# Optimization experiments

Measured on AMD Instinct MI355X. Metric: run time of the kernel, lower is better.

## Reference

```python
import jax, jax.numpy as jnp
import numpy as np

N_IN, AUX = 768, 255
NVARS = N_IN + 1 + AUX  # 1024
K, B = 32, 64
MAX_ITER = 10
PROX_LAM = 0.01


def _build_full(z, is_input):
    b = z.shape[0]
    z_full = jnp.concatenate([jnp.ones((b, 1), z.dtype), z, jnp.zeros((b, AUX), z.dtype)], axis=1)
    ii = jnp.concatenate([jnp.ones((b, 1), is_input.dtype), is_input, jnp.zeros((b, AUX), is_input.dtype)], axis=1)
    return z_full, ii


def _init_V(key, z_full, is_input_full):
    # v0: per-batch unit 'truth' direction; inputs start at -cos(pi z) v0 + sin(pi z) r
    k1, k2 = jax.random.split(key)
    v0 = jax.random.normal(k1, (B, K), jnp.float32)
    v0 = v0 / jnp.linalg.norm(v0, axis=-1, keepdims=True)
    R = jax.random.normal(k2, (B, NVARS, K), jnp.float32)
    R = R - jnp.einsum('bnk,bk->bn', R, v0)[..., None] * v0[:, None, :]
    R = R / jnp.linalg.norm(R, axis=-1, keepdims=True)  # unit, orthogonal to v0
    c = jnp.cos(jnp.pi * z_full)[..., None]
    s = jnp.sin(jnp.pi * z_full)[..., None]
    V = jnp.where(is_input_full[..., None] > 0, -c * v0[:, None, :] + s * R, R)
    V = V.at[:, 0].set(v0)  # truth variable (z=1)
    return V, v0, R


def _mix_solve(C, V, free):
    # sequential coordinate descent (Mixing method): v_i <- -g_i/||g_i||, g_i = C[i] @ V
    def step(Vc, i):
        g = jnp.einsum('j,bjk->bk', C[i], Vc)  # C_ii = 0 excludes self
        gn = jnp.maximum(jnp.linalg.norm(g, axis=-1, keepdims=True), 1e-12)
        v = jnp.where(free[:, i][:, None], -g / gn, Vc[:, i])
        return Vc.at[:, i].set(v), None

    def sweep(_, Vc):
        Vc, _ = jax.lax.scan(step, Vc, jnp.arange(1, NVARS))
        return Vc

    return jax.lax.fori_loop(0, MAX_ITER, sweep, V)


def _forward(C, z, is_input):
    z_full, ii = _build_full(z, is_input)
    free = ii == 0
    V, v0, R = _init_V(jax.random.key(42), z_full, ii)
    V = _mix_solve(C, V, free)
    cosang = jnp.clip(-jnp.einsum('bnk,bk->bn', V, v0), -1.0 + 1e-7, 1.0 - 1e-7)
    z_out = jnp.where(free, jnp.arccos(cosang) / jnp.pi, z_full)
    return z_out[:, 1:NVARS - AUX], (z_full, ii, free, V, v0, R)


def setup_inputs() -> dict:
    key = jax.random.key(0)
    kc, kz, ki = jax.random.split(key, 3)
    Ct = jax.random.normal(kc, (NVARS, NVARS), jnp.float32)
    Ct = Ct + Ct.T - 1.0
    Ct = Ct * (1.0 - jnp.eye(NVARS, dtype=jnp.float32))  # zero diagonal
    Ct = Ct * (0.5 / (NVARS * 2)) ** 0.5  # weight_normalize
    z = jax.random.uniform(kz, (B, N_IN), jnp.float32)
    is_input = jax.random.randint(ki, (B, N_IN), 0, 2).astype(jnp.int32)
    return {"C": Ct, "z": z, "is_input": is_input}


def reference(C, z, is_input):
    out, _ = _forward(C, z, is_input)
    return out
```

## Files before the change

### kernel.cpp

```cpp
#include <hip/hip_runtime.h>
#include <stdint.h>
#include <math.h>

#define NVARS 1024
#define KDIM 32
#define BATCH 64
#define NIN 768
#define MAXIT 10

#define SMEM_BYTES 156096

typedef float f32x2 __attribute__((ext_vector_type(2)));

#define PKSETUP(A0v, A1v, Dv)                                                  \
    const float4 A0_ = (A0v), A1_ = (A1v), d_ = (Dv);                          \
    f32x2 c01, c23, c45, c67, dx_, dy_, dz_, dw_;                              \
    c01.x = A0_.x; c01.y = A0_.y; c23.x = A0_.z; c23.y = A0_.w;                \
    c45.x = A1_.x; c45.y = A1_.y; c67.x = A1_.z; c67.y = A1_.w;                \
    dx_.x = d_.x;  dx_.y = d_.x;  dy_.x = d_.y;  dy_.y = d_.y;                 \
    dz_.x = d_.z;  dz_.y = d_.z;  dw_.x = d_.w;  dw_.y = d_.w;

#define PKG0                                                                   \
    Q0_0 = __builtin_elementwise_fma(c01, dx_, Q0_0);                          \
    Q1_0 = __builtin_elementwise_fma(c01, dy_, Q1_0);                          \
    Q2_0 = __builtin_elementwise_fma(c01, dz_, Q2_0);                          \
    Q3_0 = __builtin_elementwise_fma(c01, dw_, Q3_0);
#define PKG1                                                                   \
    Q0_1 = __builtin_elementwise_fma(c23, dx_, Q0_1);                          \
    Q1_1 = __builtin_elementwise_fma(c23, dy_, Q1_1);                          \
    Q2_1 = __builtin_elementwise_fma(c23, dz_, Q2_1);                          \
    Q3_1 = __builtin_elementwise_fma(c23, dw_, Q3_1);
#define PKG2                                                                   \
    Q0_2 = __builtin_elementwise_fma(c45, dx_, Q0_2);                          \
    Q1_2 = __builtin_elementwise_fma(c45, dy_, Q1_2);                          \
    Q2_2 = __builtin_elementwise_fma(c45, dz_, Q2_2);                          \
    Q3_2 = __builtin_elementwise_fma(c45, dw_, Q3_2);
#define PKG3                                                                   \
    Q0_3 = __builtin_elementwise_fma(c67, dx_, Q0_3);                          \
    Q1_3 = __builtin_elementwise_fma(c67, dy_, Q1_3);                          \
    Q2_3 = __builtin_elementwise_fma(c67, dz_, Q2_3);                          \
    Q3_3 = __builtin_elementwise_fma(c67, dw_, Q3_3);

#define PKROWR(A0v, A1v, Dv, Ra, Rb, Rc, Rd)                                   \
  { PKSETUP(A0v, A1v, Dv) PKG##Ra PKG##Rb PKG##Rc PKG##Rd }

#define PKROW(A0v, A1v, Dv) PKROWR(A0v, A1v, Dv, 0, 1, 2, 3)

__device__ __forceinline__ void tf2x32(uint32_t key0, uint32_t key1,
                                       uint32_t& x0, uint32_t& x1) {
  uint32_t ks2 = key0 ^ key1 ^ 0x1BD11BDAu;
  x0 += key0; x1 += key1;
#define TFR(r) { x0 += x1; x1 = (x1 << r) | (x1 >> (32 - r)); x1 ^= x0; }
  TFR(13) TFR(15) TFR(26) TFR(6)
  x0 += key1; x1 += ks2 + 1u;
  TFR(17) TFR(29) TFR(16) TFR(24)
  x0 += ks2;  x1 += key0 + 2u;
  TFR(13) TFR(15) TFR(26) TFR(6)
  x0 += key0; x1 += key1 + 3u;
  TFR(17) TFR(29) TFR(16) TFR(24)
  x0 += key1; x1 += ks2 + 4u;
  TFR(13) TFR(15) TFR(26) TFR(6)
  x0 += ks2;  x1 += key0 + 5u;
#undef TFR
}

__device__ __forceinline__ uint32_t pbits(uint32_t k0, uint32_t k1, uint32_t flat) {
  uint32_t x0 = 0u, x1 = flat;
  tf2x32(k0, k1, x0, x1);
  return x0 ^ x1;
}

__device__ __forceinline__ float erfinv_xla(float x) {
  float w = -log1pf(-x * x);
  float p;
  if (w < 5.0f) {
    w -= 2.5f;
    p = 2.81022636e-08f;
    p = fmaf(p, w, 3.43273939e-07f);
    p = fmaf(p, w, -3.5233877e-06f);
    p = fmaf(p, w, -4.39150654e-06f);
    p = fmaf(p, w, 0.00021858087f);
    p = fmaf(p, w, -0.00125372503f);
    p = fmaf(p, w, -0.00417768164f);
    p = fmaf(p, w, 0.246640727f);
    p = fmaf(p, w, 1.50140941f);
  } else {
    w = sqrtf(w) - 3.0f;
    p = -0.000200214257f;
    p = fmaf(p, w, 0.000100950558f);
    p = fmaf(p, w, 0.00134934322f);
    p = fmaf(p, w, -0.00367342844f);
    p = fmaf(p, w, 0.00573950773f);
    p = fmaf(p, w, -0.0076224613f);
    p = fmaf(p, w, 0.00943887047f);
    p = fmaf(p, w, 1.00167406f);
    p = fmaf(p, w, 2.83297682f);
  }
  return p * x;
}

__device__ __forceinline__ float bits_to_normal(uint32_t bits) {
  uint32_t fb = (bits >> 9) | 0x3F800000u;
  float f = __uint_as_float(fb) - 1.0f;
  const float lo = -0.99999994f;
  float u = fmaf(f, 2.0f, lo);
  u = fmaxf(lo, u);
  return 1.41421356237f * erfinv_xla(u);
}

__device__ __forceinline__ double red32d(double v) {
  v += __shfl_xor(v, 16);
  v += __shfl_xor(v, 8);
  v += __shfl_xor(v, 4);
  v += __shfl_xor(v, 2);
  v += __shfl_xor(v, 1);
  return v;
}

__device__ __forceinline__ int pop64(uint64_t& b) {
  if (b == 0ull) return -1;
  int i = (int)__builtin_ctzll(b);
  b &= b - 1ull;
  return i;
}

template <int CTRL>
__device__ __forceinline__ float dppadd(float s) {
  int v = __builtin_amdgcn_update_dpp(0, __float_as_int(s), CTRL, 0xF, 0xF, true);
  return s + __int_as_float(v);
}

#define PROW(iiL, mL, pL, cL, Ra, Rb, Rc, Rd)                                  \
  {                                                                            \
    const bool on = ((iiL) < 32) ? ((myLo >> (iiL)) & 1u)                      \
                                 : ((myHi >> ((iiL) - 32)) & 1u);              \
    if (on) {                                                                  \
      const int row = base + (iiL);                                            \
      float4 c0 = *(const float4*)(Cd + (iiL) * 64 + 8 * jgR);                 \
      float4 c1 = *(const float4*)(Cd + (iiL) * 64 + 8 * jgR + 4);             \
      float4 vold = *(const float4*)(Vs + row * 32 + 4 * kg);                  \
      const float g0 = (Q0_##pL).cL, g1 = (Q1_##pL).cL;                        \
      const float g2 = (Q2_##pL).cL, g3 = (Q3_##pL).cL;                        \
      float s = g0 * g0;                                                       \
      s = fmaf(g1, g1, s); s = fmaf(g2, g2, s); s = fmaf(g3, g3, s);           \
      s = dppadd<0xB1>(s);                   \
      s = dppadd<0x4E>(s);                   \
      s = dppadd<0x141>(s);                  \
      const float sc = fmaxf(s, 1e-24f);                                       \
      const float inv = -__builtin_amdgcn_rsqf(sc);                            \
      float4 vnew, d;                                                          \
      vnew.x = g0 * inv; d.x = vnew.x - vold.x;                                \
      vnew.y = g1 * inv; d.y = vnew.y - vold.y;                                \
      vnew.z = g2 * inv; d.z = vnew.z - vold.z;                                \
      vnew.w = g3 * inv; d.w = vnew.w - vold.w;                                \
      if (jgR == (mL)) *(float4*)(dVs + n * 32 + 4 * kg) = d;                  \
      asm volatile("" ::: "memory");                \
      if (lane == 0) progV[spar] = n + 1;                                      \
      float4 dd = *(const float4*)(dVs + n * 32 + 4 * kg);                     \
      if (jgR == (mL)) *(float4*)(Vs + row * 32 + 4 * kg) = vnew;              \
      PKROWR(c0, c1, dd, Ra, Rb, Rc, Rd);                                      \
      ++n;                                                                     \
    }                                                                          \
  }

#define PGRP(mL)                                                               \
  PROW(8 * (mL) + 0, mL, 0, x, 0, 1, 2, 3)                                     \
  PROW(8 * (mL) + 1, mL, 0, y, 1, 2, 3, 0)                                     \
  PROW(8 * (mL) + 2, mL, 1, x, 1, 2, 3, 0)                                     \
  PROW(8 * (mL) + 3, mL, 1, y, 2, 3, 0, 1)                                     \
  PROW(8 * (mL) + 4, mL, 2, x, 2, 3, 0, 1)                                     \
  PROW(8 * (mL) + 5, mL, 2, y, 3, 0, 1, 2)                                     \
  PROW(8 * (mL) + 6, mL, 3, x, 3, 0, 1, 2)                                     \
  PROW(8 * (mL) + 7, mL, 3, y, 0, 1, 2, 3)

__global__ __launch_bounds__(1024, 4) void mixnet_kernel(
    const float* __restrict__ C32, const float* __restrict__ zin,
    const int* __restrict__ is_in, float* __restrict__ out) {
  extern __shared__ char smemraw[];
  float*    Vs    = (float*)smemraw;
  float*    Cd    = (float*)(smemraw + 131072);
  float*    dVs   = (float*)(smemraw + 147456);
  uint32_t* fmask = (uint32_t*)(smemraw + 155648);
  double*   v0D   = (double*)(smemraw + 155776);
  volatile int* progV = (volatile int*)(smemraw + 156032);

  const int tid  = threadIdx.x;
  const int b    = blockIdx.x;
  const int jg   = tid >> 3;
  const int kg   = tid & 7;
  const int lane = tid & 63;
  const int wave = tid >> 6;
  const int jgR  = jg & 7;

  uint32_t myLo, myHi;
  {
    int row = tid;
    bool fr;
    if (row == 0) fr = false;
    else if (row <= NIN) fr = (is_in[b * NIN + row - 1] == 0);
    else fr = true;
    unsigned long long m = __ballot(fr);
    myLo = (uint32_t)m; myHi = (uint32_t)(m >> 32);
    if (lane == 0) { fmask[2 * wave] = myLo; fmask[2 * wave + 1] = myHi; }
  }
  if (tid == 0) { progV[0] = 0; progV[1] = 0; }

  uint32_t a0 = 0u, a1 = 0u; tf2x32(0u, 42u, a0, a1);
  uint32_t b0 = 0u, b1 = 1u; tf2x32(0u, 42u, b0, b1);

  if (tid < 32) {
    float raw = bits_to_normal(pbits(a0, a1, (uint32_t)(b * KDIM + tid)));
    double n2 = red32d((double)raw * (double)raw);
    v0D[tid] = (double)raw / sqrt(n2);
  }
  __syncthreads();

  const double PI_D = 3.14159265358979323846;

  {
    double vrow[32];
    if (tid == 0) {
#pragma unroll
      for (int t = 0; t < 16; ++t) {
        double2 w = *(const double2*)(v0D + 2 * t);
        vrow[2 * t] = w.x; vrow[2 * t + 1] = w.y;
      }
    } else {
      uint32_t base = ((uint32_t)(b * NVARS + tid)) * KDIM;
#pragma unroll
      for (int q = 0; q < 32; ++q)
        vrow[q] = (double)bits_to_normal(pbits(b0, b1, base + (uint32_t)q));
      double dot = 0.0;
#pragma unroll
      for (int t = 0; t < 16; ++t) {
        double2 w = *(const double2*)(v0D + 2 * t);
        dot += vrow[2 * t] * w.x + vrow[2 * t + 1] * w.y;
      }
#pragma unroll
      for (int t = 0; t < 16; ++t) {
        double2 w = *(const double2*)(v0D + 2 * t);
        vrow[2 * t]     -= dot * w.x;
        vrow[2 * t + 1] -= dot * w.y;
      }
      double n2 = 0.0;
#pragma unroll
      for (int q = 0; q < 32; ++q) n2 += vrow[q] * vrow[q];
      double rinv = 1.0 / sqrt(n2);
#pragma unroll
      for (int q = 0; q < 32; ++q) vrow[q] *= rinv;
      if (tid <= NIN && is_in[b * NIN + tid - 1] > 0) {
        double zf = (double)zin[b * NIN + tid - 1];
        double cc = cos(PI_D * zf), sn = sin(PI_D * zf);
#pragma unroll
        for (int t = 0; t < 16; ++t) {
          double2 w = *(const double2*)(v0D + 2 * t);
          vrow[2 * t]     = -cc * w.x + sn * vrow[2 * t];
          vrow[2 * t + 1] = -cc * w.y + sn * vrow[2 * t + 1];
        }
      }
    }
#pragma unroll
    for (int q = 0; q < 8; ++q) {
      float4 w;
      w.x = (float)vrow[4 * q];     w.y = (float)vrow[4 * q + 1];
      w.z = (float)vrow[4 * q + 2]; w.w = (float)vrow[4 * q + 3];
      *(float4*)(Vs + tid * 32 + 4 * q) = w;
    }
  }
  __syncthreads();

  f32x2 Q0_0, Q1_0, Q2_0, Q3_0, Q0_1, Q1_1, Q2_1, Q3_1;
  f32x2 Q0_2, Q1_2, Q2_2, Q3_2, Q0_3, Q1_3, Q2_3, Q3_3;
  {
    float Gj[32];
#pragma unroll
    for (int q = 0; q < 32; ++q) Gj[q] = 0.f;
    const float* Cb = C32 + (size_t)(8 * jg) * NVARS;
    for (int i = 0; i < NVARS; i += 4) {
      float4 cw[8];
#pragma unroll
      for (int l = 0; l < 8; ++l)
        cw[l] = *(const float4*)(Cb + (size_t)l * NVARS + i);
#pragma unroll
      for (int u = 0; u < 4; ++u) {
        float4 vv = *(const float4*)(Vs + (i + u) * 32 + 4 * kg);
#pragma unroll
        for (int l = 0; l < 8; ++l) {
          float cu = (u == 0) ? cw[l].x : (u == 1) ? cw[l].y
                   : (u == 2) ? cw[l].z : cw[l].w;
          Gj[l * 4 + 0] = fmaf(cu, vv.x, Gj[l * 4 + 0]);
          Gj[l * 4 + 1] = fmaf(cu, vv.y, Gj[l * 4 + 1]);
          Gj[l * 4 + 2] = fmaf(cu, vv.z, Gj[l * 4 + 2]);
          Gj[l * 4 + 3] = fmaf(cu, vv.w, Gj[l * 4 + 3]);
        }
      }
    }
    Q0_0.x = Gj[0];  Q0_0.y = Gj[4];  Q1_0.x = Gj[1];  Q1_0.y = Gj[5];
    Q2_0.x = Gj[2];  Q2_0.y = Gj[6];  Q3_0.x = Gj[3];  Q3_0.y = Gj[7];
    Q0_1.x = Gj[8];  Q0_1.y = Gj[12]; Q1_1.x = Gj[9];  Q1_1.y = Gj[13];
    Q2_1.x = Gj[10]; Q2_1.y = Gj[14]; Q3_1.x = Gj[11]; Q3_1.y = Gj[15];
    Q0_2.x = Gj[16]; Q0_2.y = Gj[20]; Q1_2.x = Gj[17]; Q1_2.y = Gj[21];
    Q2_2.x = Gj[18]; Q2_2.y = Gj[22]; Q3_2.x = Gj[19]; Q3_2.y = Gj[23];
    Q0_3.x = Gj[24]; Q0_3.y = Gj[28]; Q1_3.x = Gj[25]; Q1_3.y = Gj[29];
    Q2_3.x = Gj[26]; Q2_3.y = Gj[30]; Q3_3.x = Gj[27]; Q3_3.y = Gj[31];
  }
  __syncthreads();

  int spar = 0;
  for (int it = 0; it < MAXIT; ++it) {
    for (int g = 0; g < 16; ++g) {
      {
        int r = tid >> 4, c4 = (tid & 15) << 2;
        float4 cc = *(const float4*)(C32 + (size_t)(64 * g + r) * NVARS
                                     + 64 * g + c4);
        *(float4*)(Cd + r * 64 + c4) = cc;
      }
      const uint32_t fl = fmask[2 * g], fh = fmask[2 * g + 1];
      if (wave == g && lane == 0) progV[spar ^ 1] = 0;
      __syncthreads();

      if (wave == g) {
        __builtin_amdgcn_s_setprio(3);
        int n = 0;
        const int base = 64 * g;
        PGRP(0) PGRP(1) PGRP(2) PGRP(3)
        PGRP(4) PGRP(5) PGRP(6) PGRP(7)
        __builtin_amdgcn_s_setprio(0);
      } else {
        uint64_t pb = ((uint64_t)fh << 32) | (uint64_t)fl;
        const int cnt = (int)__builtin_popcountll(pb);
        float4 cp0[4], cp1[4];
#pragma unroll
        for (int s2 = 0; s2 < 4; ++s2) {
          int r = pop64(pb);
          if (r >= 0) {
            const float* p = C32 + (size_t)(64 * g + r) * NVARS + 8 * jg;
            cp0[s2] = *(const float4*)p; cp1[s2] = *(const float4*)(p + 4);
          }
        }
        int n2 = 0;
        while (n2 < cnt) {
          const int hi = (n2 + 4 < cnt) ? n2 + 4 : cnt;
          while (progV[spar] < hi) __builtin_amdgcn_s_sleep(8);
          if (hi == n2 + 4) {
            float4 dq0 = *(const float4*)(dVs + (n2 + 0) * 32 + 4 * kg);
            float4 dq1 = *(const float4*)(dVs + (n2 + 1) * 32 + 4 * kg);
            float4 dq2 = *(const float4*)(dVs + (n2 + 2) * 32 + 4 * kg);
            float4 dq3 = *(const float4*)(dVs + (n2 + 3) * 32 + 4 * kg);
            PKROW(cp0[0], cp1[0], dq0);
            PKROW(cp0[1], cp1[1], dq1);
            PKROW(cp0[2], cp1[2], dq2);
            PKROW(cp0[3], cp1[3], dq3);
          } else {
#pragma unroll
            for (int s2 = 0; s2 < 4; ++s2) {
              if (n2 + s2 < hi) {
                float4 dv = *(const float4*)(dVs + (n2 + s2) * 32 + 4 * kg);
                PKROW(cp0[s2], cp1[s2], dv);
              }
            }
          }
#pragma unroll
          for (int s2 = 0; s2 < 4; ++s2) {
            int r = pop64(pb);
            if (r >= 0) {
              const float* p = C32 + (size_t)(64 * g + r) * NVARS + 8 * jg;
              cp0[s2] = *(const float4*)p; cp1[s2] = *(const float4*)(p + 4);
            }
          }
          n2 = hi;
        }
      }
      spar ^= 1;
      __syncthreads();
    }
  }

  if (tid >= 1 && tid <= NIN) {
    bool fr = (fmask[tid >> 5] >> (tid & 31)) & 1u;
    float zo;
    if (fr) {
      double dot = 0.0;
#pragma unroll
      for (int t = 0; t < 16; ++t) {
        double2 w = *(const double2*)(v0D + 2 * t);
        dot += (double)Vs[tid * 32 + 2 * t] * w.x
             + (double)Vs[tid * 32 + 2 * t + 1] * w.y;
      }
      double ca = fmin(fmax(-dot, -1.0 + 1e-7), 1.0 - 1e-7);
      zo = (float)(acos(ca) / PI_D);
    } else {
      zo = zin[b * NIN + tid - 1];
    }
    out[b * NIN + tid - 1] = zo;
  }
}

extern "C" void kernel_launch(void* const* d_in, const int* in_sizes, int n_in,
                              void* d_out, int out_size, void* d_ws, size_t ws_size,
                              hipStream_t stream) {
  const float* C        = (const float*)d_in[0];
  const float* z        = (const float*)d_in[1];
  const int*   is_input = (const int*)d_in[2];
  float*       out      = (float*)d_out;
  (void)d_ws; (void)ws_size;

  (void)hipFuncSetAttribute((const void*)mixnet_kernel,
                            hipFuncAttributeMaxDynamicSharedMemorySize,
                            SMEM_BYTES);

  mixnet_kernel<<<BATCH, 1024, SMEM_BYTES, stream>>>(C, z, is_input, out);
}
```

Baseline: 2.262 ms.

## Split V init and initial gradient matmul into separate wide-grid kernels

Moves construction of the initial V matrix and the initial G = C·V product out of the 64-block solver into two preceding kernels with 256 blocks each, writing to workspace. The solver then loads V and G from global memory instead of computing them with only 64 blocks active. This spreads the prologue across more compute units at the cost of extra launches and workspace traffic. The original fused kernel is kept as a fallback when workspace is too small.

Result: no change. 2.228 ms (-1.5%).

```diff
diff --git a/kernel.cpp b/kernel.cpp
--- a/kernel.cpp
+++ b/kernel.cpp
@@ -9,6 +9,10 @@
 #define MAXIT 10
 
 #define SMEM_BYTES 156096
+
+#define WS_V_OFF 0
+#define WS_G_OFF (64ull * 1024 * 32 * 4)
+#define WS_NEEDED (2ull * 64 * 1024 * 32 * 4)
 
 typedef float f32x2 __attribute__((ext_vector_type(2)));
 
@@ -43,7 +47,6 @@
 
 #define PKROWR(A0v, A1v, Dv, Ra, Rb, Rc, Rd)                                   \
   { PKSETUP(A0v, A1v, Dv) PKG##Ra PKG##Rb PKG##Rc PKG##Rd }
-
 #define PKROW(A0v, A1v, Dv) PKROWR(A0v, A1v, Dv, 0, 1, 2, 3)
 
 __device__ __forceinline__ void tf2x32(uint32_t key0, uint32_t key1,
@@ -130,6 +133,114 @@
   return s + __int_as_float(v);
 }
 
+__device__ __forceinline__ void build_vrow(int b, int row, const float* zin,
+                                           const int* is_in, const double* v0D,
+                                           double* vrow) {
+  const double PI_D = 3.14159265358979323846;
+  uint32_t b0 = 0u, b1 = 1u; tf2x32(0u, 42u, b0, b1);
+  if (row == 0) {
+#pragma unroll
+    for (int t = 0; t < 16; ++t) {
+      double2 w = *(const double2*)(v0D + 2 * t);
+      vrow[2 * t] = w.x; vrow[2 * t + 1] = w.y;
+    }
+  } else {
+    uint32_t base = ((uint32_t)(b * NVARS + row)) * KDIM;
+#pragma unroll
+    for (int q = 0; q < 32; ++q)
+      vrow[q] = (double)bits_to_normal(pbits(b0, b1, base + (uint32_t)q));
+    double dot = 0.0;
+#pragma unroll
+    for (int t = 0; t < 16; ++t) {
+      double2 w = *(const double2*)(v0D + 2 * t);
+      dot += vrow[2 * t] * w.x + vrow[2 * t + 1] * w.y;
+    }
+#pragma unroll
+    for (int t = 0; t < 16; ++t) {
+      double2 w = *(const double2*)(v0D + 2 * t);
+      vrow[2 * t]     -= dot * w.x;
+      vrow[2 * t + 1] -= dot * w.y;
+    }
+    double n2 = 0.0;
+#pragma unroll
+    for (int q = 0; q < 32; ++q) n2 += vrow[q] * vrow[q];
+    double rinv = 1.0 / sqrt(n2);
+#pragma unroll
+    for (int q = 0; q < 32; ++q) vrow[q] *= rinv;
+    if (row <= NIN && is_in[b * NIN + row - 1] > 0) {
+      double zf = (double)zin[b * NIN + row - 1];
+      double cc = cos(PI_D * zf), sn = sin(PI_D * zf);
+#pragma unroll
+      for (int t = 0; t < 16; ++t) {
+        double2 w = *(const double2*)(v0D + 2 * t);
+        vrow[2 * t]     = -cc * w.x + sn * vrow[2 * t];
+        vrow[2 * t + 1] = -cc * w.y + sn * vrow[2 * t + 1];
+      }
+    }
+  }
+}
+
+__global__ __launch_bounds__(256) void mixnet_v(
+    const float* __restrict__ zin, const int* __restrict__ is_in,
+    float* __restrict__ Vw) {
+  __shared__ double v0D[32];
+  const int tid = threadIdx.x;
+  const int b = blockIdx.x >> 2, q = blockIdx.x & 3;
+  const int row = q * 256 + tid;
+
+  uint32_t a0 = 0u, a1 = 0u; tf2x32(0u, 42u, a0, a1);
+  if (tid < 32) {
+    float raw = bits_to_normal(pbits(a0, a1, (uint32_t)(b * KDIM + tid)));
+    double n2 = red32d((double)raw * (double)raw);
+    v0D[tid] = (double)raw / sqrt(n2);
+  }
+  __syncthreads();
+
+  double vrow[32];
+  build_vrow(b, row, zin, is_in, v0D, vrow);
+#pragma unroll
+  for (int qq = 0; qq < 8; ++qq) {
+    float4 w;
+    w.x = (float)vrow[4 * qq];     w.y = (float)vrow[4 * qq + 1];
+    w.z = (float)vrow[4 * qq + 2]; w.w = (float)vrow[4 * qq + 3];
+    *(float4*)(Vw + (size_t)(b * NVARS + row) * 32 + 4 * qq) = w;
+  }
+}
+
+__global__ __launch_bounds__(1024) void mixnet_g(
+    const float* __restrict__ C32, const float* __restrict__ Vw,
+    float* __restrict__ Gw) {
+  const int tid = threadIdx.x;
+  const int b = blockIdx.x >> 2, q = blockIdx.x & 3;
+  const int jg2 = tid >> 3, kg = tid & 7;
+  const int r0 = q * 256 + 2 * jg2;
+
+  const float* Cb0 = C32 + (size_t)r0 * NVARS;
+  const float* Cb1 = C32 + (size_t)(r0 + 1) * NVARS;
+  const float* Vb  = Vw + (size_t)b * NVARS * 32;
+
+  float G0 = 0.f, G1 = 0.f, G2 = 0.f, G3 = 0.f;
+  float G4 = 0.f, G5 = 0.f, G6 = 0.f, G7 = 0.f;
+  for (int i = 0; i < NVARS; i += 4) {
+    float4 c0 = *(const float4*)(Cb0 + i);
+    float4 c1 = *(const float4*)(Cb1 + i);
+#pragma unroll
+    for (int u = 0; u < 4; ++u) {
+      float4 vv = *(const float4*)(Vb + (size_t)(i + u) * 32 + 4 * kg);
+      float cu0 = (u == 0) ? c0.x : (u == 1) ? c0.y : (u == 2) ? c0.z : c0.w;
+      float cu1 = (u == 0) ? c1.x : (u == 1) ? c1.y : (u == 2) ? c1.z : c1.w;
+      G0 = fmaf(cu0, vv.x, G0); G1 = fmaf(cu0, vv.y, G1);
+      G2 = fmaf(cu0, vv.z, G2); G3 = fmaf(cu0, vv.w, G3);
+      G4 = fmaf(cu1, vv.x, G4); G5 = fmaf(cu1, vv.y, G5);
+      G6 = fmaf(cu1, vv.z, G6); G7 = fmaf(cu1, vv.w, G7);
+    }
+  }
+  float4 w0; w0.x = G0; w0.y = G1; w0.z = G2; w0.w = G3;
+  float4 w1; w1.x = G4; w1.y = G5; w1.z = G6; w1.w = G7;
+  *(float4*)(Gw + (size_t)(b * NVARS + r0) * 32 + 4 * kg)     = w0;
+  *(float4*)(Gw + (size_t)(b * NVARS + r0 + 1) * 32 + 4 * kg) = w1;
+}
+
 #define PROW(iiL, mL, pL, cL, Ra, Rb, Rc, Rd)                                  \
   {                                                                            \
     const bool on = ((iiL) < 32) ? ((myLo >> (iiL)) & 1u)                      \
@@ -143,9 +254,9 @@
       const float g2 = (Q2_##pL).cL, g3 = (Q3_##pL).cL;                        \
       float s = g0 * g0;                                                       \
       s = fmaf(g1, g1, s); s = fmaf(g2, g2, s); s = fmaf(g3, g3, s);           \
-      s = dppadd<0xB1>(s);                   \
-      s = dppadd<0x4E>(s);                   \
-      s = dppadd<0x141>(s);                  \
+      s = dppadd<0xB1>(s);                                                     \
+      s = dppadd<0x4E>(s);                                                     \
+      s = dppadd<0x141>(s);                                                    \
       const float sc = fmaxf(s, 1e-24f);                                       \
       const float inv = -__builtin_amdgcn_rsqf(sc);                            \
       float4 vnew, d;                                                          \
@@ -154,7 +265,7 @@
       vnew.z = g2 * inv; d.z = vnew.z - vold.z;                                \
       vnew.w = g3 * inv; d.w = vnew.w - vold.w;                                \
       if (jgR == (mL)) *(float4*)(dVs + n * 32 + 4 * kg) = d;                  \
-      asm volatile("" ::: "memory");                \
+      asm volatile("" ::: "memory");                                           \
       if (lane == 0) progV[spar] = n + 1;                                      \
       float4 dd = *(const float4*)(dVs + n * 32 + 4 * kg);                     \
       if (jgR == (mL)) *(float4*)(Vs + row * 32 + 4 * kg) = vnew;              \
@@ -173,9 +284,10 @@
   PROW(8 * (mL) + 6, mL, 3, x, 3, 0, 1, 2)                                     \
   PROW(8 * (mL) + 7, mL, 3, y, 0, 1, 2, 3)
 
-__global__ __launch_bounds__(1024, 4) void mixnet_kernel(
+__global__ __launch_bounds__(1024, 4) void mixnet_solve(
     const float* __restrict__ C32, const float* __restrict__ zin,
-    const int* __restrict__ is_in, float* __restrict__ out) {
+    const int* __restrict__ is_in, const float* __restrict__ Vw,
+    const float* __restrict__ Gw, float* __restrict__ out) {
   extern __shared__ char smemraw[];
   float*    Vs    = (float*)smemraw;
   float*    Cd    = (float*)(smemraw + 131072);
@@ -206,103 +318,39 @@
   if (tid == 0) { progV[0] = 0; progV[1] = 0; }
 
   uint32_t a0 = 0u, a1 = 0u; tf2x32(0u, 42u, a0, a1);
-  uint32_t b0 = 0u, b1 = 1u; tf2x32(0u, 42u, b0, b1);
-
   if (tid < 32) {
     float raw = bits_to_normal(pbits(a0, a1, (uint32_t)(b * KDIM + tid)));
     double n2 = red32d((double)raw * (double)raw);
     v0D[tid] = (double)raw / sqrt(n2);
   }
-  __syncthreads();
-
-  const double PI_D = 3.14159265358979323846;
 
   {
-    double vrow[32];
-    if (tid == 0) {
-#pragma unroll
-      for (int t = 0; t < 16; ++t) {
-        double2 w = *(const double2*)(v0D + 2 * t);
-        vrow[2 * t] = w.x; vrow[2 * t + 1] = w.y;
-      }
-    } else {
-      uint32_t base = ((uint32_t)(b * NVARS + tid)) * KDIM;
-#pragma unroll
-      for (int q = 0; q < 32; ++q)
-        vrow[q] = (double)bits_to_normal(pbits(b0, b1, base + (uint32_t)q));
-      double dot = 0.0;
-#pragma unroll
-      for (int t = 0; t < 16; ++t) {
-        double2 w = *(const double2*)(v0D + 2 * t);
-        dot += vrow[2 * t] * w.x + vrow[2 * t + 1] * w.y;
-      }
-#pragma unroll
-      for (int t = 0; t < 16; ++t) {
-        double2 w = *(const double2*)(v0D + 2 * t);
-        vrow[2 * t]     -= dot * w.x;
-        vrow[2 * t + 1] -= dot * w.y;
-      }
-      double n2 = 0.0;
-#pragma unroll
-      for (int q = 0; q < 32; ++q) n2 += vrow[q] * vrow[q];
-      double rinv = 1.0 / sqrt(n2);
-#pragma unroll
-      for (int q = 0; q < 32; ++q) vrow[q] *= rinv;
-      if (tid <= NIN && is_in[b * NIN + tid - 1] > 0) {
-        double zf = (double)zin[b * NIN + tid - 1];
-        double cc = cos(PI_D * zf), sn = sin(PI_D * zf);
-#pragma unroll
-        for (int t = 0; t < 16; ++t) {
-          double2 w = *(const double2*)(v0D + 2 * t);
-          vrow[2 * t]     = -cc * w.x + sn * vrow[2 * t];
-          vrow[2 * t + 1] = -cc * w.y + sn * vrow[2 * t + 1];
-        }
-      }
-    }
-#pragma unroll
-    for (int q = 0; q < 8; ++q) {
-      float4 w;
-      w.x = (float)vrow[4 * q];     w.y = (float)vrow[4 * q + 1];
-      w.z = (float)vrow[4 * q + 2]; w.w = (float)vrow[4 * q + 3];
-      *(float4*)(Vs + tid * 32 + 4 * q) = w;
-    }
-  }
-  __syncthreads();
+    const float* vp = Vw + (size_t)(b * NVARS + tid) * 32;
+#pragma unroll
+    for (int qq = 0; qq < 8; ++qq)
+      *(float4*)(Vs + tid * 32 + 4 * qq) = *(const float4*)(vp + 4 * qq);
+  }
 
   f32x2 Q0_0, Q1_0, Q2_0, Q3_0, Q0_1, Q1_1, Q2_1, Q3_1;
   f32x2 Q0_2, Q1_2, Q2_2, Q3_2, Q0_3, Q1_3, Q2_3, Q3_3;
   {
-    float Gj[32];
-#pragma unroll
-    for (int q = 0; q < 32; ++q) Gj[q] = 0.f;
-    const float* Cb = C32 + (size_t)(8 * jg) * NVARS;
-    for (int i = 0; i < NVARS; i += 4) {
-      float4 cw[8];
-#pragma unroll
-      for (int l = 0; l < 8; ++l)
-        cw[l] = *(const float4*)(Cb + (size_t)l * NVARS + i);
-#pragma unroll
-      for (int u = 0; u < 4; ++u) {
-        float4 vv = *(const float4*)(Vs + (i + u) * 32 + 4 * kg);
-#pragma unroll
-        for (int l = 0; l < 8; ++l) {
-          float cu = (u == 0) ? cw[l].x : (u == 1) ? cw[l].y
-                   : (u == 2) ? cw[l].z : cw[l].w;
-          Gj[l * 4 + 0] = fmaf(cu, vv.x, Gj[l * 4 + 0]);
-          Gj[l * 4 + 1] = fmaf(cu, vv.y, Gj[l * 4 + 1]);
-          Gj[l * 4 + 2] = fmaf(cu, vv.z, Gj[l * 4 + 2]);
-          Gj[l * 4 + 3] = fmaf(cu, vv.w, Gj[l * 4 + 3]);
-        }
-      }
-    }
-    Q0_0.x = Gj[0];  Q0_0.y = Gj[4];  Q1_0.x = Gj[1];  Q1_0.y = Gj[5];
-    Q2_0.x = Gj[2];  Q2_0.y = Gj[6];  Q3_0.x = Gj[3];  Q3_0.y = Gj[7];
-    Q0_1.x = Gj[8];  Q0_1.y = Gj[12]; Q1_1.x = Gj[9];  Q1_1.y = Gj[13];
-    Q2_1.x = Gj[10]; Q2_1.y = Gj[14]; Q3_1.x = Gj[11]; Q3_1.y = Gj[15];
-    Q0_2.x = Gj[16]; Q0_2.y = Gj[20]; Q1_2.x = Gj[17]; Q1_2.y = Gj[21];
-    Q2_2.x = Gj[18]; Q2_2.y = Gj[22]; Q3_2.x = Gj[19]; Q3_2.y = Gj[23];
-    Q0_3.x = Gj[24]; Q0_3.y = Gj[28]; Q1_3.x = Gj[25]; Q1_3.y = Gj[29];
-    Q2_3.x = Gj[26]; Q2_3.y = Gj[30]; Q3_3.x = Gj[27]; Q3_3.y = Gj[31];
+    const float* gp = Gw + (size_t)(b * NVARS + 8 * jg) * 32 + 4 * kg;
+    float4 g0 = *(const float4*)(gp + 0 * 32);
+    float4 g1 = *(const float4*)(gp + 1 * 32);
+    float4 g2 = *(const float4*)(gp + 2 * 32);
+    float4 g3 = *(const float4*)(gp + 3 * 32);
+    float4 g4 = *(const float4*)(gp + 4 * 32);
+    float4 g5 = *(const float4*)(gp + 5 * 32);
+    float4 g6 = *(const float4*)(gp + 6 * 32);
+    float4 g7 = *(const float4*)(gp + 7 * 32);
+    Q0_0.x = g0.x; Q0_0.y = g1.x; Q1_0.x = g0.y; Q1_0.y = g1.y;
+    Q2_0.x = g0.z; Q2_0.y = g1.z; Q3_0.x = g0.w; Q3_0.y = g1.w;
+    Q0_1.x = g2.x; Q0_1.y = g3.x; Q1_1.x = g2.y; Q1_1.y = g3.y;
+    Q2_1.x = g2.z; Q2_1.y = g3.z; Q3_1.x = g2.w; Q3_1.y = g3.w;
+    Q0_2.x = g4.x; Q0_2.y = g5.x; Q1_2.x = g4.y; Q1_2.y = g5.y;
+    Q2_2.x = g4.z; Q2_2.y = g5.z; Q3_2.x = g4.w; Q3_2.y = g5.w;
+    Q0_3.x = g6.x; Q0_3.y = g7.x; Q1_3.x = g6.y; Q1_3.y = g7.y;
+    Q2_3.x = g6.z; Q2_3.y = g7.z; Q3_3.x = g6.w; Q3_3.y = g7.w;
   }
   __syncthreads();
 
@@ -376,6 +424,188 @@
     }
   }
 
+  const double PI_D = 3.14159265358979323846;
+  if (tid >= 1 && tid <= NIN) {
+    bool fr = (fmask[tid >> 5] >> (tid & 31)) & 1u;
+    float zo;
+    if (fr) {
+      double dot = 0.0;
+#pragma unroll
+      for (int t = 0; t < 16; ++t) {
+        double2 w = *(const double2*)(v0D + 2 * t);
+        dot += (double)Vs[tid * 32 + 2 * t] * w.x
+             + (double)Vs[tid * 32 + 2 * t + 1] * w.y;
+      }
+      double ca = fmin(fmax(-dot, -1.0 + 1e-7), 1.0 - 1e-7);
+      zo = (float)(acos(ca) / PI_D);
+    } else {
+      zo = zin[b * NIN + tid - 1];
+    }
+    out[b * NIN + tid - 1] = zo;
+  }
+}
+
+__global__ __launch_bounds__(1024, 4) void mixnet_kernel(
+    const float* __restrict__ C32, const float* __restrict__ zin,
+    const int* __restrict__ is_in, float* __restrict__ out) {
+  extern __shared__ char smemraw[];
+  float*    Vs    = (float*)smemraw;
+  float*    Cd    = (float*)(smemraw + 131072);
+  float*    dVs   = (float*)(smemraw + 147456);
+  uint32_t* fmask = (uint32_t*)(smemraw + 155648);
+  double*   v0D   = (double*)(smemraw + 155776);
+  volatile int* progV = (volatile int*)(smemraw + 156032);
+
+  const int tid  = threadIdx.x;
+  const int b    = blockIdx.x;
+  const int jg   = tid >> 3;
+  const int kg   = tid & 7;
+  const int lane = tid & 63;
+  const int wave = tid >> 6;
+  const int jgR  = jg & 7;
+
+  uint32_t myLo, myHi;
+  {
+    int row = tid;
+    bool fr;
+    if (row == 0) fr = false;
+    else if (row <= NIN) fr = (is_in[b * NIN + row - 1] == 0);
+    else fr = true;
+    unsigned long long m = __ballot(fr);
+    myLo = (uint32_t)m; myHi = (uint32_t)(m >> 32);
+    if (lane == 0) { fmask[2 * wave] = myLo; fmask[2 * wave + 1] = myHi; }
+  }
+  if (tid == 0) { progV[0] = 0; progV[1] = 0; }
+
+  uint32_t a0 = 0u, a1 = 0u; tf2x32(0u, 42u, a0, a1);
+  if (tid < 32) {
+    float raw = bits_to_normal(pbits(a0, a1, (uint32_t)(b * KDIM + tid)));
+    double n2 = red32d((double)raw * (double)raw);
+    v0D[tid] = (double)raw / sqrt(n2);
+  }
+  __syncthreads();
+
+  {
+    double vrow[32];
+    build_vrow(b, tid, zin, is_in, v0D, vrow);
+#pragma unroll
+    for (int q = 0; q < 8; ++q) {
+      float4 w;
+      w.x = (float)vrow[4 * q];     w.y = (float)vrow[4 * q + 1];
+      w.z = (float)vrow[4 * q + 2]; w.w = (float)vrow[4 * q + 3];
+      *(float4*)(Vs + tid * 32 + 4 * q) = w;
+    }
+  }
+  __syncthreads();
+
+  f32x2 Q0_0, Q1_0, Q2_0, Q3_0, Q0_1, Q1_1, Q2_1, Q3_1;
+  f32x2 Q0_2, Q1_2, Q2_2, Q3_2, Q0_3, Q1_3, Q2_3, Q3_3;
+  {
+    float Gj[32];
+#pragma unroll
+    for (int q = 0; q < 32; ++q) Gj[q] = 0.f;
+    const float* Cb = C32 + (size_t)(8 * jg) * NVARS;
+    for (int i = 0; i < NVARS; i += 4) {
+      float4 cw[8];
+#pragma unroll
+      for (int l = 0; l < 8; ++l)
+        cw[l] = *(const float4*)(Cb + (size_t)l * NVARS + i);
+#pragma unroll
+      for (int u = 0; u < 4; ++u) {
+        float4 vv = *(const float4*)(Vs + (i + u) * 32 + 4 * kg);
+#pragma unroll
+        for (int l = 0; l < 8; ++l) {
+          float cu = (u == 0) ? cw[l].x : (u == 1) ? cw[l].y
+                   : (u == 2) ? cw[l].z : cw[l].w;
+          Gj[l * 4 + 0] = fmaf(cu, vv.x, Gj[l * 4 + 0]);
+          Gj[l * 4 + 1] = fmaf(cu, vv.y, Gj[l * 4 + 1]);
+          Gj[l * 4 + 2] = fmaf(cu, vv.z, Gj[l * 4 + 2]);
+          Gj[l * 4 + 3] = fmaf(cu, vv.w, Gj[l * 4 + 3]);
+        }
+      }
+    }
+    Q0_0.x = Gj[0];  Q0_0.y = Gj[4];  Q1_0.x = Gj[1];  Q1_0.y = Gj[5];
+    Q2_0.x = Gj[2];  Q2_0.y = Gj[6];  Q3_0.x = Gj[3];  Q3_0.y = Gj[7];
+    Q0_1.x = Gj[8];  Q0_1.y = Gj[12]; Q1_1.x = Gj[9];  Q1_1.y = Gj[13];
+    Q2_1.x = Gj[10]; Q2_1.y = Gj[14]; Q3_1.x = Gj[11]; Q3_1.y = Gj[15];
+    Q0_2.x = Gj[16]; Q0_2.y = Gj[20]; Q1_2.x = Gj[17]; Q1_2.y = Gj[21];
+    Q2_2.x = Gj[18]; Q2_2.y = Gj[22]; Q3_2.x = Gj[19]; Q3_2.y = Gj[23];
+    Q0_3.x = Gj[24]; Q0_3.y = Gj[28]; Q1_3.x = Gj[25]; Q1_3.y = Gj[29];
+    Q2_3.x = Gj[26]; Q2_3.y = Gj[30]; Q3_3.x = Gj[27]; Q3_3.y = Gj[31];
+  }
+  __syncthreads();
+
+  int spar = 0;
+  for (int it = 0; it < MAXIT; ++it) {
+    for (int g = 0; g < 16; ++g) {
+      {
+        int r = tid >> 4, c4 = (tid & 15) << 2;
+        float4 cc = *(const float4*)(C32 + (size_t)(64 * g + r) * NVARS
+                                     + 64 * g + c4);
+        *(float4*)(Cd + r * 64 + c4) = cc;
+      }
+      const uint32_t fl = fmask[2 * g], fh = fmask[2 * g + 1];
+      if (wave == g && lane == 0) progV[spar ^ 1] = 0;
+      __syncthreads();
+
+      if (wave == g) {
+        __builtin_amdgcn_s_setprio(3);
+        int n = 0;
+        const int base = 64 * g;
+        PGRP(0) PGRP(1) PGRP(2) PGRP(3)
+        PGRP(4) PGRP(5) PGRP(6) PGRP(7)
+        __builtin_amdgcn_s_setprio(0);
+      } else {
+        uint64_t pb = ((uint64_t)fh << 32) | (uint64_t)fl;
+        const int cnt = (int)__builtin_popcountll(pb);
+        float4 cp0[4], cp1[4];
+#pragma unroll
+        for (int s2 = 0; s2 < 4; ++s2) {
+          int r = pop64(pb);
+          if (r >= 0) {
+            const float* p = C32 + (size_t)(64 * g + r) * NVARS + 8 * jg;
+            cp0[s2] = *(const float4*)p; cp1[s2] = *(const float4*)(p + 4);
+          }
+        }
+        int n2 = 0;
+        while (n2 < cnt) {
+          const int hi = (n2 + 4 < cnt) ? n2 + 4 : cnt;
+          while (progV[spar] < hi) __builtin_amdgcn_s_sleep(8);
+          if (hi == n2 + 4) {
+            float4 dq0 = *(const float4*)(dVs + (n2 + 0) * 32 + 4 * kg);
+            float4 dq1 = *(const float4*)(dVs + (n2 + 1) * 32 + 4 * kg);
+            float4 dq2 = *(const float4*)(dVs + (n2 + 2) * 32 + 4 * kg);
+            float4 dq3 = *(const float4*)(dVs + (n2 + 3) * 32 + 4 * kg);
+            PKROW(cp0[0], cp1[0], dq0);
+            PKROW(cp0[1], cp1[1], dq1);
+            PKROW(cp0[2], cp1[2], dq2);
+            PKROW(cp0[3], cp1[3], dq3);
+          } else {
+#pragma unroll
+            for (int s2 = 0; s2 < 4; ++s2) {
+              if (n2 + s2 < hi) {
+                float4 dv = *(const float4*)(dVs + (n2 + s2) * 32 + 4 * kg);
+                PKROW(cp0[s2], cp1[s2], dv);
+              }
+            }
+          }
+#pragma unroll
+          for (int s2 = 0; s2 < 4; ++s2) {
+            int r = pop64(pb);
+            if (r >= 0) {
+              const float* p = C32 + (size_t)(64 * g + r) * NVARS + 8 * jg;
+              cp0[s2] = *(const float4*)p; cp1[s2] = *(const float4*)(p + 4);
+            }
+          }
+          n2 = hi;
+        }
+      }
+      spar ^= 1;
+      __syncthreads();
+    }
+  }
+
+  const double PI_D = 3.14159265358979323846;
   if (tid >= 1 && tid <= NIN) {
     bool fr = (fmask[tid >> 5] >> (tid & 31)) & 1u;
     float zo;
@@ -403,11 +633,21 @@
   const float* z        = (const float*)d_in[1];
   const int*   is_input = (const int*)d_in[2];
   float*       out      = (float*)d_out;
-  (void)d_ws; (void)ws_size;
-
+
+  (void)hipFuncSetAttribute((const void*)mixnet_solve,
+                            hipFuncAttributeMaxDynamicSharedMemorySize,
+                            SMEM_BYTES);
   (void)hipFuncSetAttribute((const void*)mixnet_kernel,
                             hipFuncAttributeMaxDynamicSharedMemorySize,
                             SMEM_BYTES);
 
-  mixnet_kernel<<<BATCH, 1024, SMEM_BYTES, stream>>>(C, z, is_input, out);
-}
+  if (d_ws != nullptr && ws_size >= WS_NEEDED) {
+    float* Vw = (float*)((char*)d_ws + WS_V_OFF);
+    float* Gw = (float*)((char*)d_ws + WS_G_OFF);
+    mixnet_v<<<256, 256, 0, stream>>>(z, is_input, Vw);
+    mixnet_g<<<256, 1024, 0, stream>>>(C, Vw, Gw);
+    mixnet_solve<<<BATCH, 1024, SMEM_BYTES, stream>>>(C, z, is_input, Vw, Gw, out);
+  } else {
+    mixnet_kernel<<<BATCH, 1024, SMEM_BYTES, stream>>>(C, z, is_input, out);
+  }
+}
```
